# Kernel optimization log

Hardware: AMD Instinct MI355X
Metric: run time of the kernel (lower is better)

## Reference

```python
import jax, jax.numpy as jnp
import numpy as np

B, S, D = 4, 2048, 1024
DFF = 512
E = 16
TOP_K = 2
N_SHARED = 2
FUSED_DFF = DFF * N_SHARED


def setup_inputs() -> dict:
    key = jax.random.key(0)
    ks = jax.random.split(key, 16)
    sc_d = 1.0 / np.sqrt(D)
    sc_f = 1.0 / np.sqrt(DFF)
    sc_sf = 1.0 / np.sqrt(FUSED_DFF)
    inp = {
        "x": jax.random.normal(ks[0], (B, S, D), dtype=jnp.float32),
        "gate_w": jax.random.uniform(ks[1], (E, D), dtype=jnp.float32, minval=-sc_d, maxval=sc_d),
        "expert_bias": jnp.zeros((E,), dtype=jnp.float32),
        # routed experts (SwiGLU): w1,w3: [E, DFF, D], w2: [E, D, DFF]
        "w1": jax.random.uniform(ks[2], (E, DFF, D), dtype=jnp.float32, minval=-sc_d, maxval=sc_d),
        "b1": jax.random.uniform(ks[3], (E, DFF), dtype=jnp.float32, minval=-sc_d, maxval=sc_d),
        "w3": jax.random.uniform(ks[4], (E, DFF, D), dtype=jnp.float32, minval=-sc_d, maxval=sc_d),
        "b3": jax.random.uniform(ks[5], (E, DFF), dtype=jnp.float32, minval=-sc_d, maxval=sc_d),
        "w2": jax.random.uniform(ks[6], (E, D, DFF), dtype=jnp.float32, minval=-sc_f, maxval=sc_f),
        "b2": jax.random.uniform(ks[7], (E, D), dtype=jnp.float32, minval=-sc_f, maxval=sc_f),
        # fused shared experts: d_model -> 2*d_ff -> d_model
        "sw1": jax.random.uniform(ks[8], (FUSED_DFF, D), dtype=jnp.float32, minval=-sc_d, maxval=sc_d),
        "sb1": jax.random.uniform(ks[9], (FUSED_DFF,), dtype=jnp.float32, minval=-sc_d, maxval=sc_d),
        "sw3": jax.random.uniform(ks[10], (FUSED_DFF, D), dtype=jnp.float32, minval=-sc_d, maxval=sc_d),
        "sb3": jax.random.uniform(ks[11], (FUSED_DFF,), dtype=jnp.float32, minval=-sc_d, maxval=sc_d),
        "sw2": jax.random.uniform(ks[12], (D, FUSED_DFF), dtype=jnp.float32, minval=-sc_sf, maxval=sc_sf),
        "sb2": jax.random.uniform(ks[13], (D,), dtype=jnp.float32, minval=-sc_sf, maxval=sc_sf),
    }
    return inp


def reference(x, gate_w, expert_bias, w1, b1, w2, b2, w3, b3,
              sw1, sb1, sw2, sb2, sw3, sb3):
    Bv, Sv, Dv = x.shape
    xf = x.reshape(-1, Dv)                                  # [T, D]
    # --- Gate (sigmoid scores, top-k over bias-adjusted logits) ---
    logits = xf @ gate_w.T                                  # [T, E]
    scores = jax.nn.sigmoid(logits)
    biased = logits + expert_bias.astype(logits.dtype)[None, :]
    _, topk_idx = jax.lax.top_k(biased, TOP_K)              # [T, K]
    topk_w = jnp.take_along_axis(scores, topk_idx, axis=-1) # [T, K]
    topk_w = topk_w / (topk_w.sum(-1, keepdims=True) + 1e-10)
    # dense per-token per-expert combine weight (zero for unselected) [T, E]
    gatew = (jax.nn.one_hot(topk_idx, E, dtype=xf.dtype) * topk_w[..., None]).sum(1)
    # --- Routed experts: equivalent to sort/dispatch/grouped-GEMM/combine ---
    y = jnp.zeros_like(xf)
    for e in range(E):
        h = jax.nn.silu(xf @ w1[e].T + b1[e]) * (xf @ w3[e].T + b3[e])  # [T, DFF]
        y = y + gatew[:, e:e + 1] * (h @ w2[e].T + b2[e])
    # --- Fused shared experts ---
    hs = jax.nn.silu(xf @ sw1.T + sb1) * (xf @ sw3.T + sb3)             # [T, 2*DFF]
    y = y + hs @ sw2.T + sb2
    return y.reshape(Bv, Sv, Dv)
```

## Files before the change

kernel.cpp:

```cpp
#include <hip/hip_runtime.h>
#include <cstdint>
#include <cstddef>

#define DEV static __device__ __forceinline__

constexpr int TT   = 8192;
constexpr int DD   = 1024;
constexpr int DFF  = 512;
constexpr int NE   = 16;
constexpr int FDFF = 1024;
constexpr int NSLOT = TT * 2;
constexpr int NSLOT_PAD = NSLOT + NE * 128;
constexpr int MAXT = NSLOT / 128 + NE;
constexpr int HB   = 64;

constexpr size_t XB_OFF   = 0;
constexpr size_t HS_OFF   = XB_OFF  + (size_t)TT * DD * 2;
constexpr size_t HR_OFF   = HS_OFF  + (size_t)TT * FDFF * 2;
constexpr size_t W1B_OFF  = HR_OFF  + (size_t)NSLOT_PAD * DFF * 2;
constexpr size_t W3B_OFF  = W1B_OFF + (size_t)NE * DFF * DD * 2;
constexpr size_t W2B_OFF  = W3B_OFF + (size_t)NE * DFF * DD * 2;
constexpr size_t SW1B_OFF = W2B_OFF + (size_t)NE * DD * DFF * 2;
constexpr size_t SW3B_OFF = SW1B_OFF + (size_t)FDFF * DD * 2;
constexpr size_t SW2B_OFF = SW3B_OFF + (size_t)FDFF * DD * 2;
constexpr size_t TKI_OFF  = SW2B_OFF + (size_t)DD * FDFF * 2;
constexpr size_t TKW_OFF  = TKI_OFF + (size_t)NSLOT * 4;
constexpr size_t STOK_OFF = TKW_OFF + (size_t)NSLOT * 4;
constexpr size_t SWT_OFF  = STOK_OFF + (size_t)NSLOT_PAD * 4;
constexpr size_t LRK_OFF  = SWT_OFF + (size_t)NSLOT_PAD * 4;
constexpr size_t BCN_OFF  = LRK_OFF + (size_t)NSLOT * 4;
constexpr size_t BB_OFF   = BCN_OFF + (size_t)HB * NE * 4;
constexpr size_t OFS_OFF  = BB_OFF + (size_t)HB * NE * 4;
constexpr size_t TEX_OFF  = OFS_OFF + 128;
constexpr size_t TM0_OFF  = TEX_OFF + (size_t)MAXT * 4;

typedef __bf16 bf16x8 __attribute__((ext_vector_type(8)));
typedef float  floatx4 __attribute__((ext_vector_type(4)));
typedef unsigned short u16t;

DEV unsigned f2bf2(float lo, float hi) {
    unsigned a = __builtin_bit_cast(unsigned, lo);
    unsigned b = __builtin_bit_cast(unsigned, hi);
    a += 0x7FFFu + ((a >> 16) & 1u);
    b += 0x7FFFu + ((b >> 16) & 1u);
    return (a >> 16) | (b & 0xFFFF0000u);
}
DEV u16t f2bf1(float f) {
    unsigned u = __builtin_bit_cast(unsigned, f);
    u += 0x7FFFu + ((u >> 16) & 1u);
    return (u16t)(u >> 16);
}
DEV uint4 pack8(float4 a, float4 b) {
    uint4 r;
    r.x = f2bf2(a.x, a.y); r.y = f2bf2(a.z, a.w);
    r.z = f2bf2(b.x, b.y); r.w = f2bf2(b.z, b.w);
    return r;
}
DEV floatx4 mfma16(bf16x8 a, bf16x8 b, floatx4 c) {
    return __builtin_amdgcn_mfma_f32_16x16x32_bf16(a, b, c, 0, 0, 0);
}
DEV void glds16(const u16t* g, u16t* l) {
    __builtin_amdgcn_global_load_lds(
        (const __attribute__((address_space(1))) unsigned int*)g,
        (__attribute__((address_space(3))) unsigned int*)l, 16, 0, 0);
}
DEV float dot4(float4 a, float4 b) { return a.x*b.x + a.y*b.y + a.z*b.z + a.w*b.w; }

__global__ __launch_bounds__(256) void k_cvtw(
        const float* __restrict__ w1, const float* __restrict__ w3, const float* __restrict__ w2,
        const float* __restrict__ sw1, const float* __restrict__ sw3, const float* __restrict__ sw2,
        u16t* __restrict__ w1b, u16t* __restrict__ w3b, u16t* __restrict__ w2b,
        u16t* __restrict__ sw1b, u16t* __restrict__ sw3b, u16t* __restrict__ sw2b) {
    int b = blockIdx.x;
    const float* src; u16t* dst; size_t base;
    if      (b < 4096)  { src = w1;  dst = w1b;  base = (size_t)b * 2048; }
    else if (b < 8192)  { src = w3;  dst = w3b;  base = (size_t)(b - 4096) * 2048; }
    else if (b < 12288) { src = w2;  dst = w2b;  base = (size_t)(b - 8192) * 2048; }
    else if (b < 12800) { src = sw1; dst = sw1b; base = (size_t)(b - 12288) * 2048; }
    else if (b < 13312) { src = sw3; dst = sw3b; base = (size_t)(b - 12800) * 2048; }
    else                { src = sw2; dst = sw2b; base = (size_t)(b - 13312) * 2048; }
    size_t i = base + (size_t)threadIdx.x * 8;
    float4 a = *(const float4*)(src + i);
    float4 c = *(const float4*)(src + i + 4);
    *(uint4*)(dst + i) = pack8(a, c);
}

__global__ __launch_bounds__(256) void k_cvtx(const float* __restrict__ x, u16t* __restrict__ xb) {
    size_t i = ((size_t)blockIdx.x * 256 + threadIdx.x) * 8;
    float4 a = *(const float4*)(x + i);
    float4 b = *(const float4*)(x + i + 4);
    *(uint4*)(xb + i) = pack8(a, b);
}

__global__ __launch_bounds__(256) void k_gate(const float* __restrict__ x,
                                              const float* __restrict__ gw,
                                              const float* __restrict__ eb,
                                              int* __restrict__ tki, float* __restrict__ tkw) {
    const int tid = threadIdx.x;
    const int wave = tid >> 6, lane = tid & 63;
    const int tok0 = blockIdx.x * 16 + wave * 4;
    float acc[4][16];
#pragma unroll
    for (int t = 0; t < 4; t++)
#pragma unroll
        for (int e = 0; e < 16; e++) acc[t][e] = 0.f;
#pragma unroll
    for (int i = 0; i < 4; i++) {
        const int d = i * 256 + lane * 4;
        float4 xv[4];
#pragma unroll
        for (int t = 0; t < 4; t++) xv[t] = *(const float4*)(x + (size_t)(tok0 + t) * DD + d);
#pragma unroll
        for (int e = 0; e < 16; e++) {
            float4 wv = *(const float4*)(gw + (size_t)e * DD + d);
#pragma unroll
            for (int t = 0; t < 4; t++) acc[t][e] += dot4(xv[t], wv);
        }
    }
#pragma unroll
    for (int t = 0; t < 4; t++)
#pragma unroll
        for (int e = 0; e < 16; e++) {
            float v = acc[t][e];
            v += __shfl_xor(v, 1);  v += __shfl_xor(v, 2);  v += __shfl_xor(v, 4);
            v += __shfl_xor(v, 8);  v += __shfl_xor(v, 16); v += __shfl_xor(v, 32);
            acc[t][e] = v;
        }
    if (lane == 0) {
        float ebs[16];
#pragma unroll
        for (int e = 0; e < 16; e++) ebs[e] = eb[e];
#pragma unroll
        for (int t = 0; t < 4; t++) {
            float b0 = -1e30f, b1v = -1e30f, l0 = 0.f, l1 = 0.f;
            int i0 = 0, i1 = 0;
#pragma unroll
            for (int e = 0; e < 16; e++) {
                float lv = acc[t][e];
                float bl = lv + ebs[e];
                if (bl > b0)       { b1v = b0; i1 = i0; l1 = l0; b0 = bl; i0 = e; l0 = lv; }
                else if (bl > b1v) { b1v = bl; i1 = e; l1 = lv; }
            }
            float s0 = 1.f / (1.f + expf(-l0));
            float s1 = 1.f / (1.f + expf(-l1));
            float dn = s0 + s1 + 1e-10f;
            int tok = tok0 + t;
            tki[tok * 2] = i0; tki[tok * 2 + 1] = i1;
            tkw[tok * 2] = s0 / dn; tkw[tok * 2 + 1] = s1 / dn;
        }
    }
}

__global__ __launch_bounds__(256) void k_hist(const int* __restrict__ tki,
                                              int* __restrict__ lrank, int* __restrict__ bcnt) {
    __shared__ int h[NE];
    const int tid = threadIdx.x;
    if (tid < NE) h[tid] = 0;
    __syncthreads();
    int idx = blockIdx.x * 256 + tid;
    int e = tki[idx];
    lrank[idx] = atomicAdd(&h[e], 1);
    __syncthreads();
    if (tid < NE) bcnt[blockIdx.x * NE + tid] = h[tid];
}

__global__ void k_scan(const int* __restrict__ bcnt, int* __restrict__ offs,
                       int* __restrict__ bb, int* __restrict__ texp, int* __restrict__ tm0) {
    __shared__ int cntS[NE], offS[NE];
    const int tid = threadIdx.x;
    if (tid < NE) {
        int s = 0;
#pragma unroll
        for (int b = 0; b < HB; b++) s += bcnt[b * NE + tid];
        cntS[tid] = s;
    }
    __syncthreads();
    if (tid == 0) {
        int off = 0, t = 0;
        for (int e = 0; e < NE; e++) {
            offS[e] = off; offs[e] = off;
            int nt = (cntS[e] + 127) >> 7;
            for (int i = 0; i < nt; i++) { texp[t] = e; tm0[t] = off + i * 128; t++; }
            off += nt * 128;
        }
        offs[NE] = off;
        for (; t < MAXT; t++) texp[t] = -1;
    }
    __syncthreads();
    if (tid < NE) {
        int run = offS[tid];
        for (int b = 0; b < HB; b++) { bb[b * NE + tid] = run; run += bcnt[b * NE + tid]; }
    }
}

__global__ __launch_bounds__(256) void k_scatter(const int* __restrict__ tki,
                                                 const float* __restrict__ tkw,
                                                 const int* __restrict__ bb,
                                                 const int* __restrict__ lrank,
                                                 int* __restrict__ stok, float* __restrict__ swt) {
    int idx = blockIdx.x * 256 + threadIdx.x;
    int e = tki[idx];
    int slot = bb[blockIdx.x * NE + e] + lrank[idx];
    stok[slot] = idx >> 1;
    swt[slot] = tkw[idx];
}

__global__ __launch_bounds__(256) void k_sgemm1(const u16t* __restrict__ xb,
        const u16t* __restrict__ w1b, const float* __restrict__ sb1,
        const u16t* __restrict__ w3b, const float* __restrict__ sb3,
        u16t* __restrict__ Hs) {
    __shared__ u16t As[128 * 32], B1s[64 * 32], B3s[64 * 32];
    const int m0 = blockIdx.x * 128, n0 = blockIdx.y * 64;
    const int tid = threadIdx.x, lane = tid & 63, wid = tid >> 6;
    const int wm = (wid & 1) * 64, wn = (wid >> 1) * 32;
    const int q = lane >> 4, r = lane & 15;
    const int srow = tid >> 2, scg = (tid & 3) * 8;
    floatx4 acc1[4][2], acc3[4][2];
#pragma unroll
    for (int i = 0; i < 4; i++)
#pragma unroll
        for (int j = 0; j < 2; j++) { acc1[i][j] = (floatx4)0.f; acc3[i][j] = (floatx4)0.f; }
    const u16t* a0  = xb  + (size_t)(m0 + srow) * DD + scg;
    const u16t* a1  = xb  + (size_t)(m0 + 64 + srow) * DD + scg;
    const u16t* b1g = w1b + (size_t)(n0 + srow) * DD + scg;
    const u16t* b3g = w3b + (size_t)(n0 + srow) * DD + scg;
    u16t* lA0 = As + tid * 8;
    u16t* lA1 = As + 2048 + tid * 8;
    u16t* lB1 = B1s + tid * 8;
    u16t* lB3 = B3s + tid * 8;
    for (int k0 = 0; k0 < DD; k0 += 32) {
        glds16(a0 + k0, lA0); glds16(a1 + k0, lA1);
        glds16(b1g + k0, lB1); glds16(b3g + k0, lB3);
        __syncthreads();
        bf16x8 af[4], f1[2], f3[2];
#pragma unroll
        for (int i = 0; i < 4; i++) af[i] = *(const bf16x8*)&As[(wm + i * 16 + r) * 32 + q * 8];
#pragma unroll
        for (int j = 0; j < 2; j++) {
            f1[j] = *(const bf16x8*)&B1s[(wn + j * 16 + r) * 32 + q * 8];
            f3[j] = *(const bf16x8*)&B3s[(wn + j * 16 + r) * 32 + q * 8];
        }
#pragma unroll
        for (int i = 0; i < 4; i++)
#pragma unroll
            for (int j = 0; j < 2; j++) {
                acc1[i][j] = mfma16(af[i], f1[j], acc1[i][j]);
                acc3[i][j] = mfma16(af[i], f3[j], acc3[i][j]);
            }
        __syncthreads();
    }
    float s1v[2], s3v[2];
#pragma unroll
    for (int j = 0; j < 2; j++) {
        int col = n0 + wn + j * 16 + r;
        s1v[j] = sb1[col]; s3v[j] = sb3[col];
    }
#pragma unroll
    for (int i = 0; i < 4; i++)
#pragma unroll
        for (int j = 0; j < 2; j++)
#pragma unroll
            for (int g = 0; g < 4; g++) {
                int row = m0 + wm + i * 16 + q * 4 + g;
                int col = n0 + wn + j * 16 + r;
                float z1 = acc1[i][j][g] + s1v[j];
                float z3 = acc3[i][j][g] + s3v[j];
                float h = (z1 / (1.f + __expf(-z1))) * z3;
                Hs[(size_t)row * FDFF + col] = f2bf1(h);
            }
}

__global__ __launch_bounds__(256) void k_sgemm2(const u16t* __restrict__ Hs,
        const u16t* __restrict__ sw2b, const float* __restrict__ sb2,
        float* __restrict__ out) {
    __shared__ u16t As[128 * 32], Bs[128 * 32];
    const int m0 = blockIdx.x * 128, n0 = blockIdx.y * 128;
    const int tid = threadIdx.x, lane = tid & 63, wid = tid >> 6;
    const int wm = (wid & 1) * 64, wn = (wid >> 1) * 64;
    const int q = lane >> 4, r = lane & 15;
    const int srow = tid >> 2, scg = (tid & 3) * 8;
    floatx4 acc[4][4];
#pragma unroll
    for (int i = 0; i < 4; i++)
#pragma unroll
        for (int j = 0; j < 4; j++) acc[i][j] = (floatx4)0.f;
    const u16t* a0 = Hs + (size_t)(m0 + srow) * FDFF + scg;
    const u16t* a1 = Hs + (size_t)(m0 + 64 + srow) * FDFF + scg;
    const u16t* b0 = sw2b + (size_t)(n0 + srow) * FDFF + scg;
    const u16t* b1 = sw2b + (size_t)(n0 + 64 + srow) * FDFF + scg;
    u16t* lA0 = As + tid * 8;       u16t* lA1 = As + 2048 + tid * 8;
    u16t* lB0 = Bs + tid * 8;       u16t* lB1 = Bs + 2048 + tid * 8;
    for (int k0 = 0; k0 < FDFF; k0 += 32) {
        glds16(a0 + k0, lA0); glds16(a1 + k0, lA1);
        glds16(b0 + k0, lB0); glds16(b1 + k0, lB1);
        __syncthreads();
        bf16x8 af[4], bf[4];
#pragma unroll
        for (int i = 0; i < 4; i++) af[i] = *(const bf16x8*)&As[(wm + i * 16 + r) * 32 + q * 8];
#pragma unroll
        for (int j = 0; j < 4; j++) bf[j] = *(const bf16x8*)&Bs[(wn + j * 16 + r) * 32 + q * 8];
#pragma unroll
        for (int i = 0; i < 4; i++)
#pragma unroll
            for (int j = 0; j < 4; j++) acc[i][j] = mfma16(af[i], bf[j], acc[i][j]);
        __syncthreads();
    }
    float bv[4];
#pragma unroll
    for (int j = 0; j < 4; j++) bv[j] = sb2[n0 + wn + j * 16 + r];
#pragma unroll
    for (int i = 0; i < 4; i++)
#pragma unroll
        for (int j = 0; j < 4; j++)
#pragma unroll
            for (int g = 0; g < 4; g++) {
                int row = m0 + wm + i * 16 + q * 4 + g;
                int col = n0 + wn + j * 16 + r;
                out[(size_t)row * DD + col] = acc[i][j][g] + bv[j];
            }
}

__global__ __launch_bounds__(256) void k_rgemm1(const u16t* __restrict__ xb,
        const u16t* __restrict__ w1b, const float* __restrict__ b1,
        const u16t* __restrict__ w3b, const float* __restrict__ b3,
        const int* __restrict__ stok,
        const int* __restrict__ texp, const int* __restrict__ tm0,
        u16t* __restrict__ Hr) {
    const int te = texp[blockIdx.x];
    if (te < 0) return;
    const int m0 = tm0[blockIdx.x], n0 = blockIdx.y * 64;
    __shared__ u16t As[128 * 32], B1s[64 * 32], B3s[64 * 32];
    __shared__ int toksS[128];
    const int tid = threadIdx.x, lane = tid & 63, wid = tid >> 6;
    const int wm = (wid & 1) * 64, wn = (wid >> 1) * 32;
    const int q = lane >> 4, r = lane & 15;
    const int srow = tid >> 2, scg = (tid & 3) * 8;
    if (tid < 128) { int t = stok[m0 + tid]; toksS[tid] = t < 0 ? 0 : t; }
    __syncthreads();
    floatx4 acc1[4][2], acc3[4][2];
#pragma unroll
    for (int i = 0; i < 4; i++)
#pragma unroll
        for (int j = 0; j < 2; j++) { acc1[i][j] = (floatx4)0.f; acc3[i][j] = (floatx4)0.f; }
    const u16t* a0  = xb + (size_t)toksS[srow] * DD + scg;
    const u16t* a1  = xb + (size_t)toksS[64 + srow] * DD + scg;
    const u16t* b1g = w1b + (size_t)te * DFF * DD + (size_t)(n0 + srow) * DD + scg;
    const u16t* b3g = w3b + (size_t)te * DFF * DD + (size_t)(n0 + srow) * DD + scg;
    const float* b1e = b1 + (size_t)te * DFF;
    const float* b3e = b3 + (size_t)te * DFF;
    u16t* lA0 = As + tid * 8;
    u16t* lA1 = As + 2048 + tid * 8;
    u16t* lB1 = B1s + tid * 8;
    u16t* lB3 = B3s + tid * 8;
    for (int k0 = 0; k0 < DD; k0 += 32) {
        glds16(a0 + k0, lA0); glds16(a1 + k0, lA1);
        glds16(b1g + k0, lB1); glds16(b3g + k0, lB3);
        __syncthreads();
        bf16x8 af[4], f1[2], f3[2];
#pragma unroll
        for (int i = 0; i < 4; i++) af[i] = *(const bf16x8*)&As[(wm + i * 16 + r) * 32 + q * 8];
#pragma unroll
        for (int j = 0; j < 2; j++) {
            f1[j] = *(const bf16x8*)&B1s[(wn + j * 16 + r) * 32 + q * 8];
            f3[j] = *(const bf16x8*)&B3s[(wn + j * 16 + r) * 32 + q * 8];
        }
#pragma unroll
        for (int i = 0; i < 4; i++)
#pragma unroll
            for (int j = 0; j < 2; j++) {
                acc1[i][j] = mfma16(af[i], f1[j], acc1[i][j]);
                acc3[i][j] = mfma16(af[i], f3[j], acc3[i][j]);
            }
        __syncthreads();
    }
    float s1v[2], s3v[2];
#pragma unroll
    for (int j = 0; j < 2; j++) {
        int col = n0 + wn + j * 16 + r;
        s1v[j] = b1e[col]; s3v[j] = b3e[col];
    }
#pragma unroll
    for (int i = 0; i < 4; i++)
#pragma unroll
        for (int j = 0; j < 2; j++)
#pragma unroll
            for (int g = 0; g < 4; g++) {
                int slot = m0 + wm + i * 16 + q * 4 + g;
                int col = n0 + wn + j * 16 + r;
                float z1 = acc1[i][j][g] + s1v[j];
                float z3 = acc3[i][j][g] + s3v[j];
                float h = (z1 / (1.f + __expf(-z1))) * z3;
                Hr[(size_t)slot * DFF + col] = f2bf1(h);
            }
}

__global__ __launch_bounds__(256) void k_rgemm2(const u16t* __restrict__ Hr,
        const u16t* __restrict__ w2b, const float* __restrict__ b2,
        const int* __restrict__ stok, const float* __restrict__ swt,
        const int* __restrict__ texp, const int* __restrict__ tm0,
        float* __restrict__ out) {
    const int te = texp[blockIdx.x];
    if (te < 0) return;
    const int m0 = tm0[blockIdx.x], n0 = blockIdx.y * 128;
    __shared__ u16t As[128 * 32], Bs[128 * 32];
    __shared__ int toksR[128];
    __shared__ float swtL[128];
    const int tid = threadIdx.x, lane = tid & 63, wid = tid >> 6;
    const int wm = (wid & 1) * 64, wn = (wid >> 1) * 64;
    const int q = lane >> 4, r = lane & 15;
    const int srow = tid >> 2, scg = (tid & 3) * 8;
    if (tid < 128) { toksR[tid] = stok[m0 + tid]; swtL[tid] = swt[m0 + tid]; }
    floatx4 acc[4][4];
#pragma unroll
    for (int i = 0; i < 4; i++)
#pragma unroll
        for (int j = 0; j < 4; j++) acc[i][j] = (floatx4)0.f;
    const u16t* a0 = Hr + (size_t)(m0 + srow) * DFF + scg;
    const u16t* a1 = Hr + (size_t)(m0 + 64 + srow) * DFF + scg;
    const u16t* b0 = w2b + (size_t)te * DD * DFF + (size_t)(n0 + srow) * DFF + scg;
    const u16t* b1 = w2b + (size_t)te * DD * DFF + (size_t)(n0 + 64 + srow) * DFF + scg;
    const float* b2e = b2 + (size_t)te * DD;
    u16t* lA0 = As + tid * 8;       u16t* lA1 = As + 2048 + tid * 8;
    u16t* lB0 = Bs + tid * 8;       u16t* lB1 = Bs + 2048 + tid * 8;
    for (int k0 = 0; k0 < DFF; k0 += 32) {
        glds16(a0 + k0, lA0); glds16(a1 + k0, lA1);
        glds16(b0 + k0, lB0); glds16(b1 + k0, lB1);
        __syncthreads();
        bf16x8 af[4], bf[4];
#pragma unroll
        for (int i = 0; i < 4; i++) af[i] = *(const bf16x8*)&As[(wm + i * 16 + r) * 32 + q * 8];
#pragma unroll
        for (int j = 0; j < 4; j++) bf[j] = *(const bf16x8*)&Bs[(wn + j * 16 + r) * 32 + q * 8];
#pragma unroll
        for (int i = 0; i < 4; i++)
#pragma unroll
            for (int j = 0; j < 4; j++) acc[i][j] = mfma16(af[i], bf[j], acc[i][j]);
        __syncthreads();
    }
    float bv[4];
#pragma unroll
    for (int j = 0; j < 4; j++) bv[j] = b2e[n0 + wn + j * 16 + r];
#pragma unroll
    for (int i = 0; i < 4; i++)
#pragma unroll
        for (int g = 0; g < 4; g++) {
            int rowl = wm + i * 16 + q * 4 + g;
            int tk = toksR[rowl];
            if (tk >= 0) {
                float gwv = swtL[rowl];
#pragma unroll
                for (int j = 0; j < 4; j++) {
                    int col = n0 + wn + j * 16 + r;
                    atomicAdd(out + (size_t)tk * DD + col, gwv * (acc[i][j][g] + bv[j]));
                }
            }
        }
}

extern "C" void kernel_launch(void* const* d_in, const int* in_sizes, int n_in,
                              void* d_out, int out_size, void* d_ws, size_t ws_size,
                              hipStream_t stream) {
    const float* x   = (const float*)d_in[0];
    const float* gw  = (const float*)d_in[1];
    const float* eb  = (const float*)d_in[2];
    const float* w1  = (const float*)d_in[3];
    const float* b1  = (const float*)d_in[4];
    const float* w3  = (const float*)d_in[5];
    const float* b3  = (const float*)d_in[6];
    const float* w2  = (const float*)d_in[7];
    const float* b2  = (const float*)d_in[8];
    const float* sw1 = (const float*)d_in[9];
    const float* sb1 = (const float*)d_in[10];
    const float* sw3 = (const float*)d_in[11];
    const float* sb3 = (const float*)d_in[12];
    const float* sw2 = (const float*)d_in[13];
    const float* sb2 = (const float*)d_in[14];
    float* out = (float*)d_out;
    char* ws = (char*)d_ws;

    u16t*  xb   = (u16t*)(ws + XB_OFF);
    u16t*  Hs   = (u16t*)(ws + HS_OFF);
    u16t*  Hr   = (u16t*)(ws + HR_OFF);
    u16t*  w1b  = (u16t*)(ws + W1B_OFF);
    u16t*  w3b  = (u16t*)(ws + W3B_OFF);
    u16t*  w2b  = (u16t*)(ws + W2B_OFF);
    u16t*  sw1b = (u16t*)(ws + SW1B_OFF);
    u16t*  sw3b = (u16t*)(ws + SW3B_OFF);
    u16t*  sw2b = (u16t*)(ws + SW2B_OFF);
    int*   tki  = (int*)(ws + TKI_OFF);
    float* tkw  = (float*)(ws + TKW_OFF);
    int*   stok = (int*)(ws + STOK_OFF);
    float* swt  = (float*)(ws + SWT_OFF);
    int*   lrank = (int*)(ws + LRK_OFF);
    int*   bcnt = (int*)(ws + BCN_OFF);
    int*   bb   = (int*)(ws + BB_OFF);
    int*   offs = (int*)(ws + OFS_OFF);
    int*   texp = (int*)(ws + TEX_OFF);
    int*   tm0  = (int*)(ws + TM0_OFF);

    hipMemsetAsync(stok, 0xFF, (size_t)NSLOT_PAD * 4, stream);

    k_cvtw<<<13824, 256, 0, stream>>>(w1, w3, w2, sw1, sw3, sw2, w1b, w3b, w2b, sw1b, sw3b, sw2b);
    k_cvtx<<<4096, 256, 0, stream>>>(x, xb);
    k_gate<<<512, 256, 0, stream>>>(x, gw, eb, tki, tkw);
    k_hist<<<HB, 256, 0, stream>>>(tki, lrank, bcnt);
    k_scan<<<1, 64, 0, stream>>>(bcnt, offs, bb, texp, tm0);
    k_scatter<<<HB, 256, 0, stream>>>(tki, tkw, bb, lrank, stok, swt);

    k_sgemm1<<<dim3(TT / 128, FDFF / 64), 256, 0, stream>>>(xb, sw1b, sb1, sw3b, sb3, Hs);
    k_sgemm2<<<dim3(TT / 128, DD / 128), 256, 0, stream>>>(Hs, sw2b, sb2, out);
    k_rgemm1<<<dim3(MAXT, DFF / 64), 256, 0, stream>>>(xb, w1b, b1, w3b, b3, stok, texp, tm0, Hr);
    k_rgemm2<<<dim3(MAXT, DD / 128), 256, 0, stream>>>(Hr, w2b, b2, stok, swt, texp, tm0, out);
}
```

Measured before the change: 467.6 us.

## Replace atomic combine with bf16 expert outputs gathered in shared-expert epilogue

The routed down-projection now writes per-slot bf16 outputs to a new buffer instead of doing fp32 atomicAdd scatter into the output. The shared-expert down-projection epilogue gathers each token's two slot rows via a token-to-slot map and adds the weighted sum. The kernels are reordered so routed GEMMs run before the shared ones. Separately, the x-to-bf16 conversion is folded into the gate kernel, which removes one launch and one read of x. This trades atomic contention for an extra write and read of the intermediate buffer, and routed outputs are now rounded to bf16, which adds precision loss.

```diff
diff --git a/kernel.cpp b/kernel.cpp
--- a/kernel.cpp
+++ b/kernel.cpp
@@ -17,7 +17,8 @@
 constexpr size_t XB_OFF   = 0;
 constexpr size_t HS_OFF   = XB_OFF  + (size_t)TT * DD * 2;
 constexpr size_t HR_OFF   = HS_OFF  + (size_t)TT * FDFF * 2;
-constexpr size_t W1B_OFF  = HR_OFF  + (size_t)NSLOT_PAD * DFF * 2;
+constexpr size_t YR_OFF   = HR_OFF  + (size_t)NSLOT_PAD * DFF * 2;
+constexpr size_t W1B_OFF  = YR_OFF  + (size_t)NSLOT_PAD * DD * 2;
 constexpr size_t W3B_OFF  = W1B_OFF + (size_t)NE * DFF * DD * 2;
 constexpr size_t W2B_OFF  = W3B_OFF + (size_t)NE * DFF * DD * 2;
 constexpr size_t SW1B_OFF = W2B_OFF + (size_t)NE * DD * DFF * 2;
@@ -26,8 +27,8 @@
 constexpr size_t TKI_OFF  = SW2B_OFF + (size_t)DD * FDFF * 2;
 constexpr size_t TKW_OFF  = TKI_OFF + (size_t)NSLOT * 4;
 constexpr size_t STOK_OFF = TKW_OFF + (size_t)NSLOT * 4;
-constexpr size_t SWT_OFF  = STOK_OFF + (size_t)NSLOT_PAD * 4;
-constexpr size_t LRK_OFF  = SWT_OFF + (size_t)NSLOT_PAD * 4;
+constexpr size_t TSL_OFF  = STOK_OFF + (size_t)NSLOT_PAD * 4;
+constexpr size_t LRK_OFF  = TSL_OFF + (size_t)NSLOT * 4;
 constexpr size_t BCN_OFF  = LRK_OFF + (size_t)NSLOT * 4;
 constexpr size_t BB_OFF   = BCN_OFF + (size_t)HB * NE * 4;
 constexpr size_t OFS_OFF  = BB_OFF + (size_t)HB * NE * 4;
@@ -49,6 +50,9 @@
     unsigned u = __builtin_bit_cast(unsigned, f);
     u += 0x7FFFu + ((u >> 16) & 1u);
     return (u16t)(u >> 16);
+}
+DEV float bf2f(u16t v) {
+    return __builtin_bit_cast(float, ((unsigned)v) << 16);
 }
 DEV uint4 pack8(float4 a, float4 b) {
     uint4 r;
@@ -85,17 +89,11 @@
     *(uint4*)(dst + i) = pack8(a, c);
 }
 
-__global__ __launch_bounds__(256) void k_cvtx(const float* __restrict__ x, u16t* __restrict__ xb) {
-    size_t i = ((size_t)blockIdx.x * 256 + threadIdx.x) * 8;
-    float4 a = *(const float4*)(x + i);
-    float4 b = *(const float4*)(x + i + 4);
-    *(uint4*)(xb + i) = pack8(a, b);
-}
-
 __global__ __launch_bounds__(256) void k_gate(const float* __restrict__ x,
                                               const float* __restrict__ gw,
                                               const float* __restrict__ eb,
-                                              int* __restrict__ tki, float* __restrict__ tkw) {
+                                              int* __restrict__ tki, float* __restrict__ tkw,
+                                              u16t* __restrict__ xb) {
     const int tid = threadIdx.x;
     const int wave = tid >> 6, lane = tid & 63;
     const int tok0 = blockIdx.x * 16 + wave * 4;
@@ -110,6 +108,13 @@
         float4 xv[4];
 #pragma unroll
         for (int t = 0; t < 4; t++) xv[t] = *(const float4*)(x + (size_t)(tok0 + t) * DD + d);
+#pragma unroll
+        for (int t = 0; t < 4; t++) {
+            uint2 p;
+            p.x = f2bf2(xv[t].x, xv[t].y);
+            p.y = f2bf2(xv[t].z, xv[t].w);
+            *(uint2*)(xb + (size_t)(tok0 + t) * DD + d) = p;
+        }
 #pragma unroll
         for (int e = 0; e < 16; e++) {
             float4 wv = *(const float4*)(gw + (size_t)e * DD + d);
@@ -194,15 +199,15 @@
 }
 
 __global__ __launch_bounds__(256) void k_scatter(const int* __restrict__ tki,
-                                                 const float* __restrict__ tkw,
                                                  const int* __restrict__ bb,
                                                  const int* __restrict__ lrank,
-                                                 int* __restrict__ stok, float* __restrict__ swt) {
+                                                 int* __restrict__ stok,
+                                                 int* __restrict__ tslot) {
     int idx = blockIdx.x * 256 + threadIdx.x;
     int e = tki[idx];
     int slot = bb[blockIdx.x * NE + e] + lrank[idx];
     stok[slot] = idx >> 1;
-    swt[slot] = tkw[idx];
+    tslot[idx] = slot;
 }
 
 __global__ __launch_bounds__(256) void k_sgemm1(const u16t* __restrict__ xb,
@@ -272,13 +277,19 @@
 
 __global__ __launch_bounds__(256) void k_sgemm2(const u16t* __restrict__ Hs,
         const u16t* __restrict__ sw2b, const float* __restrict__ sb2,
+        const u16t* __restrict__ Yr, const int* __restrict__ tslot,
+        const float* __restrict__ tkw,
         float* __restrict__ out) {
     __shared__ u16t As[128 * 32], Bs[128 * 32];
+    __shared__ int sl[256];
+    __shared__ float wl[256];
     const int m0 = blockIdx.x * 128, n0 = blockIdx.y * 128;
     const int tid = threadIdx.x, lane = tid & 63, wid = tid >> 6;
     const int wm = (wid & 1) * 64, wn = (wid >> 1) * 64;
     const int q = lane >> 4, r = lane & 15;
     const int srow = tid >> 2, scg = (tid & 3) * 8;
+    sl[tid] = tslot[m0 * 2 + tid];
+    wl[tid] = tkw[m0 * 2 + tid];
     floatx4 acc[4][4];
 #pragma unroll
     for (int i = 0; i < 4; i++)
@@ -311,13 +322,20 @@
 #pragma unroll
     for (int i = 0; i < 4; i++)
 #pragma unroll
-        for (int j = 0; j < 4; j++)
-#pragma unroll
-            for (int g = 0; g < 4; g++) {
-                int row = m0 + wm + i * 16 + q * 4 + g;
+        for (int g = 0; g < 4; g++) {
+            int rowl = wm + i * 16 + q * 4 + g;
+            int s0 = sl[rowl * 2], s1 = sl[rowl * 2 + 1];
+            float w0 = wl[rowl * 2], w1 = wl[rowl * 2 + 1];
+            const u16t* y0p = Yr + (size_t)s0 * DD;
+            const u16t* y1p = Yr + (size_t)s1 * DD;
+#pragma unroll
+            for (int j = 0; j < 4; j++) {
                 int col = n0 + wn + j * 16 + r;
-                out[(size_t)row * DD + col] = acc[i][j][g] + bv[j];
-            }
+                float v = acc[i][j][g] + bv[j];
+                v += w0 * bf2f(y0p[col]) + w1 * bf2f(y1p[col]);
+                out[(size_t)(m0 + rowl) * DD + col] = v;
+            }
+        }
 }
 
 __global__ __launch_bounds__(256) void k_rgemm1(const u16t* __restrict__ xb,
@@ -396,20 +414,16 @@
 
 __global__ __launch_bounds__(256) void k_rgemm2(const u16t* __restrict__ Hr,
         const u16t* __restrict__ w2b, const float* __restrict__ b2,
-        const int* __restrict__ stok, const float* __restrict__ swt,
         const int* __restrict__ texp, const int* __restrict__ tm0,
-        float* __restrict__ out) {
+        u16t* __restrict__ Yr) {
     const int te = texp[blockIdx.x];
     if (te < 0) return;
     const int m0 = tm0[blockIdx.x], n0 = blockIdx.y * 128;
     __shared__ u16t As[128 * 32], Bs[128 * 32];
-    __shared__ int toksR[128];
-    __shared__ float swtL[128];
     const int tid = threadIdx.x, lane = tid & 63, wid = tid >> 6;
     const int wm = (wid & 1) * 64, wn = (wid >> 1) * 64;
     const int q = lane >> 4, r = lane & 15;
     const int srow = tid >> 2, scg = (tid & 3) * 8;
-    if (tid < 128) { toksR[tid] = stok[m0 + tid]; swtL[tid] = swt[m0 + tid]; }
     floatx4 acc[4][4];
 #pragma unroll
     for (int i = 0; i < 4; i++)
@@ -444,15 +458,11 @@
     for (int i = 0; i < 4; i++)
 #pragma unroll
         for (int g = 0; g < 4; g++) {
-            int rowl = wm + i * 16 + q * 4 + g;
-            int tk = toksR[rowl];
-            if (tk >= 0) {
-                float gwv = swtL[rowl];
-#pragma unroll
-                for (int j = 0; j < 4; j++) {
-                    int col = n0 + wn + j * 16 + r;
-                    atomicAdd(out + (size_t)tk * DD + col, gwv * (acc[i][j][g] + bv[j]));
-                }
+            int slot = m0 + wm + i * 16 + q * 4 + g;
+#pragma unroll
+            for (int j = 0; j < 4; j++) {
+                int col = n0 + wn + j * 16 + r;
+                Yr[(size_t)slot * DD + col] = f2bf1(acc[i][j][g] + bv[j]);
             }
         }
 }
@@ -481,6 +491,7 @@
     u16t*  xb   = (u16t*)(ws + XB_OFF);
     u16t*  Hs   = (u16t*)(ws + HS_OFF);
     u16t*  Hr   = (u16t*)(ws + HR_OFF);
+    u16t*  Yr   = (u16t*)(ws + YR_OFF);
     u16t*  w1b  = (u16t*)(ws + W1B_OFF);
     u16t*  w3b  = (u16t*)(ws + W3B_OFF);
     u16t*  w2b  = (u16t*)(ws + W2B_OFF);
@@ -490,7 +501,7 @@
     int*   tki  = (int*)(ws + TKI_OFF);
     float* tkw  = (float*)(ws + TKW_OFF);
     int*   stok = (int*)(ws + STOK_OFF);
-    float* swt  = (float*)(ws + SWT_OFF);
+    int*   tslot = (int*)(ws + TSL_OFF);
     int*   lrank = (int*)(ws + LRK_OFF);
     int*   bcnt = (int*)(ws + BCN_OFF);
     int*   bb   = (int*)(ws + BB_OFF);
@@ -501,14 +512,14 @@
     hipMemsetAsync(stok, 0xFF, (size_t)NSLOT_PAD * 4, stream);
 
     k_cvtw<<<13824, 256, 0, stream>>>(w1, w3, w2, sw1, sw3, sw2, w1b, w3b, w2b, sw1b, sw3b, sw2b);
-    k_cvtx<<<4096, 256, 0, stream>>>(x, xb);
-    k_gate<<<512, 256, 0, stream>>>(x, gw, eb, tki, tkw);
+    k_gate<<<512, 256, 0, stream>>>(x, gw, eb, tki, tkw, xb);
     k_hist<<<HB, 256, 0, stream>>>(tki, lrank, bcnt);
     k_scan<<<1, 64, 0, stream>>>(bcnt, offs, bb, texp, tm0);
-    k_scatter<<<HB, 256, 0, stream>>>(tki, tkw, bb, lrank, stok, swt);
+    k_scatter<<<HB, 256, 0, stream>>>(tki, bb, lrank, stok, tslot);
+
+    k_rgemm1<<<dim3(MAXT, DFF / 64), 256, 0, stream>>>(xb, w1b, b1, w3b, b3, stok, texp, tm0, Hr);
+    k_rgemm2<<<dim3(MAXT, DD / 128), 256, 0, stream>>>(Hr, w2b, b2, texp, tm0, Yr);
 
     k_sgemm1<<<dim3(TT / 128, FDFF / 64), 256, 0, stream>>>(xb, sw1b, sb1, sw3b, sb3, Hs);
-    k_sgemm2<<<dim3(TT / 128, DD / 128), 256, 0, stream>>>(Hs, sw2b, sb2, out);
-    k_rgemm1<<<dim3(MAXT, DFF / 64), 256, 0, stream>>>(xb, w1b, b1, w3b, b3, stok, texp, tm0, Hr);
-    k_rgemm2<<<dim3(MAXT, DD / 128), 256, 0, stream>>>(Hr, w2b, b2, stok, swt, texp, tm0, out);
-}
+    k_sgemm2<<<dim3(TT / 128, DD / 128), 256, 0, stream>>>(Hs, sw2b, sb2, Yr, tslot, tkw, out);
+}
```

After: 416.6 us. 1.12x faster.
